# Kernel tuning notes

Measured on AMD Instinct MI355X. Metric: run time of the kernel, lower is better.

Reference implementation:

```python
import math
import jax, jax.numpy as jnp
import numpy as np

K = 8            # kernel_size (patch length)
OUT = 8
STRIDE = 1
PAD = 0
DEPTH = 2
N = max(OUT, K)  # n_qubits = 8
PI = math.pi


def _apply_1q(state, U, wire):
    # state: [P] + [2]*N, U: [2,2] (shared) or [P,2,2] (per-patch)
    st = jnp.moveaxis(state, wire + 1, -1)
    if U.ndim == 3:
        st = jnp.einsum('pij,p...j->p...i', U, st)
    else:
        st = jnp.einsum('ij,p...j->p...i', U, st)
    return jnp.moveaxis(st, -1, wire + 1)


def _apply_cnot(state, c, t):
    # flip target-axis amplitudes on the control=1 half
    s0, s1 = jnp.split(state, 2, axis=c + 1)
    s1 = jnp.flip(s1, axis=t + 1)
    return jnp.concatenate([s0, s1], axis=c + 1)


def _rot_matrix(phi, theta, omega):
    # PennyLane Rot(phi, theta, omega) = RZ(omega) RY(theta) RZ(phi)
    c = jnp.cos(theta / 2)
    s = jnp.sin(theta / 2)
    m00 = jnp.exp(-0.5j * (phi + omega)) * c
    m01 = -jnp.exp(0.5j * (phi - omega)) * s
    m10 = jnp.exp(-0.5j * (phi - omega)) * s
    m11 = jnp.exp(0.5j * (phi + omega)) * c
    return jnp.stack([jnp.stack([m00, m01]), jnp.stack([m10, m11])]).astype(jnp.complex64)


def setup_inputs() -> dict:
    key = jax.random.key(0)
    k1, k2, k3 = jax.random.split(key, 3)
    x = jax.random.normal(k1, (8, 1, 8192), dtype=jnp.float32)
    # TorchLayer default init for angle weights: uniform in [0, 2*pi)
    weights = jax.random.uniform(k2, (DEPTH, N, 3), dtype=jnp.float32) * (2 * PI)
    bias = jax.random.normal(k3, (OUT,), dtype=jnp.float32) * 0.01
    return {"x": x, "weights": weights, "bias": bias}


def reference(x, weights, bias):
    B, C, L = x.shape
    xp = jnp.pad(x, ((0, 0), (0, 0), (PAD, PAD)))
    Lout = (L + 2 * PAD - K) // STRIDE + 1
    idx = np.arange(Lout)[:, None] * STRIDE + np.arange(K)[None, :]  # [Lout, K]
    patches = xp[:, 0, :][:, idx]                    # [B, Lout, K]
    ang = PI * jnp.tanh(patches).reshape(-1, K)      # [P, K] encoding angles
    P = ang.shape[0]

    # batched statevector |0...0>, shape [P] + [2]*N
    state = jnp.zeros((P, 2 ** N), jnp.complex64).at[:, 0].set(1.0)
    state = state.reshape((P,) + (2,) * N)

    # AngleEmbedding: RX(angle) per qubit (qubits >= K get RX(0) = identity)
    for w in range(K):
        th = ang[:, w]
        c = jnp.cos(th / 2).astype(jnp.complex64)
        s = (-1j * jnp.sin(th / 2)).astype(jnp.complex64)
        U = jnp.stack([jnp.stack([c, s], -1), jnp.stack([s, c], -1)], -2)  # [P,2,2]
        state = _apply_1q(state, U, w)

    # StronglyEntanglingLayers: Rot on each wire, then CNOT ring with range r
    for l in range(DEPTH):
        for w in range(N):
            U = _rot_matrix(weights[l, w, 0], weights[l, w, 1], weights[l, w, 2])
            state = _apply_1q(state, U, w)
        r = (l % (N - 1)) + 1
        for w in range(N):
            state = _apply_cnot(state, w, (w + r) % N)

    probs = (state.real ** 2 + state.imag ** 2).reshape(P, 2 ** N)
    d = np.arange(2 ** N)
    # <Z_i> sign of each basis state (axis 0 of the [2]*N tensor is wire 0 = MSB)
    signs = np.stack([1.0 - 2.0 * ((d >> (N - 1 - i)) & 1) for i in range(OUT)], 0).astype(np.float32)
    e = probs @ signs.T                              # [P, OUT]
    out = (e + bias).reshape(B, Lout, OUT).transpose(0, 2, 1)  # [B, OUT, Lout]
    return out
```

## Files before the change

### kernel.cpp

```cpp
#include <hip/hip_runtime.h>
#include <hip/hip_bf16.h>


#define TOTAL_PATCHES 65480
#define LOUT 8185
#define LBATCH 8192

typedef _Float16 f16x8 __attribute__((ext_vector_type(8)));
typedef float f32x4 __attribute__((ext_vector_type(4)));

static __device__ __forceinline__ unsigned short f2h_bits(float f) {
  union { _Float16 h; unsigned short u; } v;
  v.h = (_Float16)f;
  return v.u;
}

__global__ __launch_bounds__(256) void prep_all(const float* __restrict__ x,
                                                const float* __restrict__ w,
                                                unsigned short* __restrict__ wf16,
                                                float* __restrict__ cs,
                                                float* __restrict__ sn) {
  if (blockIdx.x >= 256) {
    int e = (blockIdx.x - 256) * 256 + threadIdx.x;
    float t = tanhf(x[e]);
    float s, c;
    __sincosf(1.57079632679489662f * t, &s, &c);
    cs[e] = c;
    sn[e] = s;
    return;
  }
  __shared__ float re[256], im[256];
  const int k = blockIdx.x;
  const int t = threadIdx.x;
  re[t] = 0.f; im[t] = 0.f;
  __syncthreads();
  if (t == 0) re[k] = 1.f;
  __syncthreads();
  for (int l = 0; l < 2; ++l) {
    for (int wi = 0; wi < 8; ++wi) {
      float phi = w[(l * 8 + wi) * 3 + 0];
      float th  = w[(l * 8 + wi) * 3 + 1];
      float om  = w[(l * 8 + wi) * 3 + 2];
      float ch = cosf(0.5f * th), sh = sinf(0.5f * th);
      float aa = 0.5f * (phi + om), bb = 0.5f * (phi - om);
      float ca = cosf(aa), sa = sinf(aa), cb = cosf(bb), sb = sinf(bb);
      float m00r = ch * ca, m00i = -ch * sa;
      float m01r = -sh * cb, m01i = -sh * sb;
      float m10r = sh * cb,  m10i = -sh * sb;
      float m11r = ch * ca,  m11i = ch * sa;
      int pos = 7 - wi;
      int mask = 1 << pos;
      int lowm = mask - 1;
      if (t < 128) {
        int pp = t;
        int d0 = ((pp & ~lowm) << 1) | (pp & lowm);
        int d1 = d0 | mask;
        float a0r = re[d0], a0i = im[d0], a1r = re[d1], a1i = im[d1];
        re[d0] = m00r * a0r - m00i * a0i + m01r * a1r - m01i * a1i;
        im[d0] = m00r * a0i + m00i * a0r + m01r * a1i + m01i * a1r;
        re[d1] = m10r * a0r - m10i * a0i + m11r * a1r - m11i * a1i;
        im[d1] = m10r * a0i + m10i * a0r + m11r * a1i + m11i * a1r;
      }
      __syncthreads();
    }
    int r = (l % 7) + 1;
    for (int wi = 0; wi < 8; ++wi) {
      int c = wi, tg = (wi + r) & 7;
      int pc = 7 - c, pt = 7 - tg;
      int p1 = pc > pt ? pc : pt, p0 = pc < pt ? pc : pt;
      if (t < 64) {
        int lm0 = (1 << p0) - 1;
        int v2 = ((t & ~lm0) << 1) | (t & lm0);
        int lm1 = (1 << p1) - 1;
        int db = ((v2 & ~lm1) << 1) | (v2 & lm1);
        int d0 = db | (1 << pc);
        int d1 = d0 | (1 << pt);
        float tr = re[d0], ti = im[d0];
        re[d0] = re[d1]; im[d0] = im[d1];
        re[d1] = tr;     im[d1] = ti;
      }
      __syncthreads();
    }
  }
  int pop = __popc(k) & 3;
  for (int idx = t; idx < 512; idx += 256) {
    int n = idx;
    int d = n & 255;
    float vr = re[d], vi = im[d];
    float pr, qi;
    if (pop == 0)      { pr =  vr; qi =  vi; }
    else if (pop == 1) { pr =  vi; qi = -vr; }
    else if (pop == 2) { pr = -vr; qi = -vi; }
    else               { pr = -vi; qi =  vr; }
    float val = (n < 256) ? pr : qi;
    int off = (((k >> 5) * 32 + (n >> 4)) * 64 + ((k >> 3) & 3) * 16 + (n & 15)) * 8 + (k & 7);
    wf16[off] = f2h_bits(val);
  }
}

__global__ __launch_bounds__(512, 2) void quanv_main(
    const float* __restrict__ cs, const float* __restrict__ sn,
    const f16x8* __restrict__ wf, const float* __restrict__ bias,
    float* __restrict__ out) {
  __shared__ __align__(16) unsigned short R0[64 * 264];
  __shared__ float esm[512];
  const int tid = threadIdx.x;
  const int lane = tid & 63;
  const int wave = tid >> 6;
  const int pbase = blockIdx.x * 64;

  {
    int pl = tid & 31;
    int q = (tid >> 5) & 7;
    int s = tid >> 8;
    int patch = pbase + s * 32 + pl;
    if (patch > TOTAL_PATCHES - 1) patch = TOTAL_PATCHES - 1;
    int b = patch / LOUT;
    int l = patch - b * LOUT;
    int base = b * LBATCH + l;
    float fc[8], fs[8];
#pragma unroll
    for (int wq = 0; wq < 8; ++wq) { fc[wq] = cs[base + wq]; fs[wq] = sn[base + wq]; }
    float arr[32];
    arr[0] = ((q & 4) ? fs[0] : fc[0]) * ((q & 2) ? fs[1] : fc[1]) * ((q & 1) ? fs[2] : fc[2]);
#pragma unroll
    for (int lev = 0; lev < 5; ++lev) {
      int wq = 7 - lev;
      int sz = 1 << lev;
#pragma unroll
      for (int j = 0; j < 32; ++j) {
        if (j < sz) {
          float a = arr[j];
          arr[sz + j] = a * fs[wq];
          arr[j] = a * fc[wq];
        }
      }
    }
    int mtg = s * 2 + (pl >> 4);
    int fragbase = (q * 4 + mtg) * 64 + (pl & 15);
#pragma unroll
    for (int khalf = 0; khalf < 4; ++khalf) {
      f16x8 vH;
#pragma unroll
      for (int jj = 0; jj < 8; ++jj) vH[jj] = (_Float16)arr[khalf * 8 + jj];
      *(f16x8*)&R0[(fragbase + khalf * 16) * 8] = vH;
    }
  }
  __syncthreads();

  f32x4 acc[4][4];
#pragma unroll
  for (int i = 0; i < 4; ++i)
#pragma unroll
    for (int j = 0; j < 4; ++j) acc[i][j] = (f32x4){0.f, 0.f, 0.f, 0.f};

#pragma unroll
  for (int kc = 0; kc < 8; ++kc) {
    f16x8 af[4];
#pragma unroll
    for (int mt = 0; mt < 4; ++mt)
      af[mt] = *(const f16x8*)&R0[((kc * 4 + mt) * 64 + lane) * 8];
#pragma unroll
    for (int t4 = 0; t4 < 4; ++t4) {
      int nt = (t4 < 2) ? (wave * 2 + t4) : (16 + wave * 2 + (t4 - 2));
      f16x8 b = wf[(kc * 32 + nt) * 64 + lane];
#pragma unroll
      for (int mt = 0; mt < 4; ++mt)
        acc[mt][t4] = __builtin_amdgcn_mfma_f32_16x16x32_f16(af[mt], b, acc[mt][t4], 0, 0, 0);
    }
  }

  __syncthreads();
#pragma unroll
  for (int mt = 0; mt < 4; ++mt)
#pragma unroll
    for (int t2 = 0; t2 < 2; ++t2)
#pragma unroll
      for (int r = 0; r < 4; ++r) {
        float vr = acc[mt][t2][r], vi = acc[mt][t2 + 2][r];
        float p = vr * vr + vi * vi;
        int patch_l = mt * 16 + (lane >> 4) * 4 + r;
        int d = (wave * 2 + t2) * 16 + (lane & 15);
        R0[patch_l * 264 + d] = f2h_bits(p);
      }
  __syncthreads();

  if (wave < 4) {
    f32x4 e4 = {0.f, 0.f, 0.f, 0.f};
    int io = lane & 15;
    int plr = wave * 16 + (lane & 15);
    int hi4 = lane >> 4;
#pragma unroll
    for (int kc2 = 0; kc2 < 8; ++kc2) {
      int k0 = kc2 * 32 + hi4 * 8;
      f16x8 aH = *(const f16x8*)&R0[plr * 264 + k0];
      f16x8 b2;
#pragma unroll
      for (int bb = 0; bb < 8; ++bb) {
        _Float16 sv = (_Float16)0.f;
        if (io < 8) sv = (((k0 + bb) >> (7 - io)) & 1) ? (_Float16)(-1.f) : (_Float16)(1.f);
        b2[bb] = sv;
      }
      e4 = __builtin_amdgcn_mfma_f32_16x16x32_f16(aH, b2, e4, 0, 0, 0);
    }
    if (io < 8) {
      float bv = bias[io];
#pragma unroll
      for (int r = 0; r < 4; ++r)
        esm[io * 64 + (wave * 16 + hi4 * 4 + r)] = e4[r] + bv;
    }
  }
  __syncthreads();

  {
    int io2 = tid >> 6, pl2 = tid & 63;
    int patch = pbase + pl2;
    if (patch < TOTAL_PATCHES) {
      int b = patch / LOUT;
      int l = patch - b * LOUT;
      out[(b * 8 + io2) * LOUT + l] = esm[io2 * 64 + pl2];
    }
  }
}

extern "C" void kernel_launch(void* const* d_in, const int* in_sizes, int n_in,
                              void* d_out, int out_size, void* d_ws, size_t ws_size,
                              hipStream_t stream) {
  const float* x = (const float*)d_in[0];
  const float* w = (const float*)d_in[1];
  const float* bias = (const float*)d_in[2];
  float* out = (float*)d_out;
  char* ws = (char*)d_ws;
  unsigned short* wf16 = (unsigned short*)ws;
  float* cs = (float*)(ws + 262144);
  float* sn = (float*)(ws + 524288);

  prep_all<<<512, 256, 0, stream>>>(x, w, wf16, cs, sn);
  quanv_main<<<1024, 512, 0, stream>>>(cs, sn, (const f16x8*)wf16, bias, out);
}
```

Baseline: 39.04 us.

## Double patch tile per block to 128 and interleave cos/sin into float2

The main kernel now handles 128 patches per block with 1024 threads. Each wave owns one real/imag pair of output column tiles across eight M tiles, which halves the number of times the unitary fragments are loaded from global memory per patch. The cos and sin tables are stored interleaved as float2, so each angle needs a single load. The cost is a larger shared-memory footprint, one block per CU, more accumulator registers per thread, and half as many blocks in the grid.

```diff
diff --git a/kernel.cpp b/kernel.cpp
--- a/kernel.cpp
+++ b/kernel.cpp
@@ -18,15 +18,13 @@
 __global__ __launch_bounds__(256) void prep_all(const float* __restrict__ x,
                                                 const float* __restrict__ w,
                                                 unsigned short* __restrict__ wf16,
-                                                float* __restrict__ cs,
-                                                float* __restrict__ sn) {
+                                                float2* __restrict__ csn) {
   if (blockIdx.x >= 256) {
     int e = (blockIdx.x - 256) * 256 + threadIdx.x;
     float t = tanhf(x[e]);
     float s, c;
     __sincosf(1.57079632679489662f * t, &s, &c);
-    cs[e] = c;
-    sn[e] = s;
+    csn[e] = make_float2(c, s);
     return;
   }
   __shared__ float re[256], im[256];
@@ -98,16 +96,16 @@
   }
 }
 
-__global__ __launch_bounds__(512, 2) void quanv_main(
-    const float* __restrict__ cs, const float* __restrict__ sn,
+__global__ __launch_bounds__(1024, 1) void quanv_main(
+    const float2* __restrict__ csn,
     const f16x8* __restrict__ wf, const float* __restrict__ bias,
     float* __restrict__ out) {
-  __shared__ __align__(16) unsigned short R0[64 * 264];
-  __shared__ float esm[512];
+  __shared__ __align__(16) unsigned short R0[128 * 264];
+  __shared__ float esm[1024];
   const int tid = threadIdx.x;
   const int lane = tid & 63;
   const int wave = tid >> 6;
-  const int pbase = blockIdx.x * 64;
+  const int pbase = blockIdx.x * 128;
 
   {
     int pl = tid & 31;
@@ -120,7 +118,10 @@
     int base = b * LBATCH + l;
     float fc[8], fs[8];
 #pragma unroll
-    for (int wq = 0; wq < 8; ++wq) { fc[wq] = cs[base + wq]; fs[wq] = sn[base + wq]; }
+    for (int wq = 0; wq < 8; ++wq) {
+      float2 v = csn[base + wq];
+      fc[wq] = v.x; fs[wq] = v.y;
+    }
     float arr[32];
     arr[0] = ((q & 4) ? fs[0] : fc[0]) * ((q & 2) ? fs[1] : fc[1]) * ((q & 1) ? fs[2] : fc[2]);
 #pragma unroll
@@ -137,7 +138,7 @@
       }
     }
     int mtg = s * 2 + (pl >> 4);
-    int fragbase = (q * 4 + mtg) * 64 + (pl & 15);
+    int fragbase = (q * 8 + mtg) * 64 + (pl & 15);
 #pragma unroll
     for (int khalf = 0; khalf < 4; ++khalf) {
       f16x8 vH;
@@ -148,44 +149,42 @@
   }
   __syncthreads();
 
-  f32x4 acc[4][4];
-#pragma unroll
-  for (int i = 0; i < 4; ++i)
-#pragma unroll
-    for (int j = 0; j < 4; ++j) acc[i][j] = (f32x4){0.f, 0.f, 0.f, 0.f};
+  f32x4 acc[8][2];
+#pragma unroll
+  for (int i = 0; i < 8; ++i)
+#pragma unroll
+    for (int j = 0; j < 2; ++j) acc[i][j] = (f32x4){0.f, 0.f, 0.f, 0.f};
 
 #pragma unroll
   for (int kc = 0; kc < 8; ++kc) {
-    f16x8 af[4];
-#pragma unroll
-    for (int mt = 0; mt < 4; ++mt)
-      af[mt] = *(const f16x8*)&R0[((kc * 4 + mt) * 64 + lane) * 8];
-#pragma unroll
-    for (int t4 = 0; t4 < 4; ++t4) {
-      int nt = (t4 < 2) ? (wave * 2 + t4) : (16 + wave * 2 + (t4 - 2));
+    f16x8 af[8];
+#pragma unroll
+    for (int mt = 0; mt < 8; ++mt)
+      af[mt] = *(const f16x8*)&R0[((kc * 8 + mt) * 64 + lane) * 8];
+#pragma unroll
+    for (int t2 = 0; t2 < 2; ++t2) {
+      int nt = (t2 == 0) ? wave : (16 + wave);
       f16x8 b = wf[(kc * 32 + nt) * 64 + lane];
 #pragma unroll
-      for (int mt = 0; mt < 4; ++mt)
-        acc[mt][t4] = __builtin_amdgcn_mfma_f32_16x16x32_f16(af[mt], b, acc[mt][t4], 0, 0, 0);
-    }
-  }
-
-  __syncthreads();
-#pragma unroll
-  for (int mt = 0; mt < 4; ++mt)
-#pragma unroll
-    for (int t2 = 0; t2 < 2; ++t2)
-#pragma unroll
-      for (int r = 0; r < 4; ++r) {
-        float vr = acc[mt][t2][r], vi = acc[mt][t2 + 2][r];
-        float p = vr * vr + vi * vi;
-        int patch_l = mt * 16 + (lane >> 4) * 4 + r;
-        int d = (wave * 2 + t2) * 16 + (lane & 15);
-        R0[patch_l * 264 + d] = f2h_bits(p);
-      }
-  __syncthreads();
-
-  if (wave < 4) {
+      for (int mt = 0; mt < 8; ++mt)
+        acc[mt][t2] = __builtin_amdgcn_mfma_f32_16x16x32_f16(af[mt], b, acc[mt][t2], 0, 0, 0);
+    }
+  }
+
+  __syncthreads();
+#pragma unroll
+  for (int mt = 0; mt < 8; ++mt)
+#pragma unroll
+    for (int r = 0; r < 4; ++r) {
+      float vr = acc[mt][0][r], vi = acc[mt][1][r];
+      float p = vr * vr + vi * vi;
+      int patch_l = mt * 16 + (lane >> 4) * 4 + r;
+      int d = wave * 16 + (lane & 15);
+      R0[patch_l * 264 + d] = f2h_bits(p);
+    }
+  __syncthreads();
+
+  if (wave < 8) {
     f32x4 e4 = {0.f, 0.f, 0.f, 0.f};
     int io = lane & 15;
     int plr = wave * 16 + (lane & 15);
@@ -207,18 +206,18 @@
       float bv = bias[io];
 #pragma unroll
       for (int r = 0; r < 4; ++r)
-        esm[io * 64 + (wave * 16 + hi4 * 4 + r)] = e4[r] + bv;
+        esm[io * 128 + (wave * 16 + hi4 * 4 + r)] = e4[r] + bv;
     }
   }
   __syncthreads();
 
   {
-    int io2 = tid >> 6, pl2 = tid & 63;
+    int io2 = tid >> 7, pl2 = tid & 127;
     int patch = pbase + pl2;
     if (patch < TOTAL_PATCHES) {
       int b = patch / LOUT;
       int l = patch - b * LOUT;
-      out[(b * 8 + io2) * LOUT + l] = esm[io2 * 64 + pl2];
+      out[(b * 8 + io2) * LOUT + l] = esm[io2 * 128 + pl2];
     }
   }
 }
@@ -232,9 +231,8 @@
   float* out = (float*)d_out;
   char* ws = (char*)d_ws;
   unsigned short* wf16 = (unsigned short*)ws;
-  float* cs = (float*)(ws + 262144);
-  float* sn = (float*)(ws + 524288);
-
-  prep_all<<<512, 256, 0, stream>>>(x, w, wf16, cs, sn);
-  quanv_main<<<1024, 512, 0, stream>>>(cs, sn, (const f16x8*)wf16, bias, out);
-}
+  float2* csn = (float2*)(ws + 262144);
+
+  prep_all<<<512, 256, 0, stream>>>(x, w, wf16, csn);
+  quanv_main<<<512, 1024, 0, stream>>>(csn, (const f16x8*)wf16, bias, out);
+}
```

Result: faster. 38.15 us (-2.3%).
